# Optimization experiments

Hardware: AMD Instinct MI355X
Metric: run time of the kernel (lower is better)

The kernel has to match this reference:

```python
import jax, jax.numpy as jnp
import numpy as np

EPS = 1e-06


def setup_inputs() -> dict:
    key = jax.random.key(0)
    k1, k2, k3 = jax.random.split(key, 3)
    shape = (64, 1, 480, 640)
    pred = jax.random.normal(k1, shape, dtype=jnp.float32)
    target = jax.random.normal(k2, shape, dtype=jnp.float32)
    valid_mask = jax.random.randint(k3, shape, 0, 2).astype(jnp.bool_)
    return {"pred": pred, "target": target, "valid_mask": valid_mask}


def reference(pred, target, valid_mask):
    B = pred.shape[0]
    mask = valid_mask & jnp.isfinite(pred) & jnp.isfinite(target)
    m = mask.reshape(B, -1)                      # [B, N] bool
    # Zero out invalid entries so non-finite values cannot poison reductions.
    p = jnp.where(m, pred.reshape(B, -1), 0.0)   # [B, N]
    t = jnp.where(m, target.reshape(B, -1), 0.0)  # [B, N]
    mf = m.astype(pred.dtype)

    n = mf.sum(axis=-1)                           # valid count per sample
    sum_p = p.sum(axis=-1)
    sum_t = t.sum(axis=-1)
    sum_p2 = (p * p).sum(axis=-1)
    sum_pt = (p * t).sum(axis=-1)

    det = n * sum_p2 - sum_p * sum_p
    safe = jnp.abs(det) > EPS
    det_safe = jnp.where(safe, det, 1.0)
    a = jnp.where(safe, (n * sum_pt - sum_p * sum_t) / det_safe, 1.0)
    b = jnp.where(safe, (sum_t - a * sum_p) / jnp.maximum(n, 1.0), 0.0)

    # Masked mean absolute residual per sample.
    resid = jnp.abs(a[:, None] * p + b[:, None] - t) * mf
    per_sample = resid.sum(axis=-1) / jnp.maximum(n, 1.0)

    include = (n >= 2.0).astype(pred.dtype)      # samples with < 2 valid px skipped
    cnt = include.sum()
    loss = jnp.where(cnt > 0, (per_sample * include).sum() / jnp.maximum(cnt, 1.0), 0.0)
    return loss
```

## Files before the change

kernel.cpp:

```cpp
#include <hip/hip_runtime.h>

#define B_SAMPLES 64
#define F4PS      76800
#define BPS       30
#define F4PB      2560
#define TPB       256
#define ITERS     10
#define WPB       4
#define EPS_DET   1e-6f

typedef __attribute__((address_space(3))) void       lds_void;
typedef const __attribute__((address_space(1))) void gbl_void;

__device__ __forceinline__ bool finitef(float x) {
    return (__float_as_uint(x) & 0x7f800000u) != 0x7f800000u;
}

__device__ __forceinline__ bool detect_byte_layout(const void* mask, int base4,
                                                   int* sflag) {
    const uint4* m16 =
        (const uint4*)((const unsigned char*)mask + (size_t)base4 * 4);
    uint4 m = m16[threadIdx.x];
    unsigned v = (m.x | m.y | m.z | m.w) & 0xffffff00u;
    if (threadIdx.x == 0) *sflag = 0;
    __syncthreads();
    if (__any(v != 0) && (threadIdx.x & 63) == 0) *sflag = 1;
    __syncthreads();
    return *sflag != 0;
}

__device__ __forceinline__ void stage3(const float4* gp, const float4* gt,
                                       const unsigned* gm,
                                       unsigned char* lbuf) {
    __builtin_amdgcn_global_load_lds((gbl_void*)gp, (lds_void*)lbuf, 16, 0, 0);
    __builtin_amdgcn_global_load_lds((gbl_void*)gt, (lds_void*)(lbuf + 1024),
                                     16, 0, 0);
    __builtin_amdgcn_global_load_lds((gbl_void*)gm, (lds_void*)(lbuf + 2048),
                                     4, 0, 0);
}

__global__ void
sums_kernel(const float* __restrict__ pred, const float* __restrict__ target,
            const void* __restrict__ mask, float* __restrict__ partials) {
    const int s   = blockIdx.x / BPS;
    const int sub = blockIdx.x % BPS;
    const int base4 = s * F4PS + sub * F4PB;
    const int tid = threadIdx.x, lane = tid & 63, w = tid >> 6;

    __shared__ __align__(16) unsigned char stg[WPB][2][2304];
    __shared__ float red[WPB][5];
    __shared__ int sflag;

    const bool byteLayout = detect_byte_layout(mask, base4, &sflag);

    const float4* p4 = (const float4*)pred;
    const float4* t4 = (const float4*)target;

    float n = 0.f, sp = 0.f, st = 0.f, sp2 = 0.f, spt = 0.f;
    auto accum = [&](float p, float t, bool mv) {
        bool ok = mv && finitef(p) && finitef(t);
        float pv = ok ? p : 0.f;
        float tv = ok ? t : 0.f;
        n   += ok ? 1.f : 0.f;
        sp  += pv;
        st  += tv;
        sp2 += pv * pv;
        spt += pv * tv;
    };

    if (byteLayout) {
        const unsigned* m4 = (const unsigned*)mask;
        unsigned char* buf0 = &stg[w][0][0];
        unsigned char* buf1 = &stg[w][1][0];
        const int i0 = base4 + w * 64 + lane;
        stage3(p4 + i0, t4 + i0, m4 + i0, buf0);
#pragma unroll
        for (int t = 0; t < ITERS; ++t) {
            unsigned char* cur = (t & 1) ? buf1 : buf0;
            unsigned char* nxt = (t & 1) ? buf0 : buf1;
            if (t < ITERS - 1) {
                const int i4 = i0 + (t + 1) * TPB;
                stage3(p4 + i4, t4 + i4, m4 + i4, nxt);
                __builtin_amdgcn_sched_barrier(0);
                asm volatile("s_waitcnt vmcnt(3)" ::: "memory");
            } else {
                __builtin_amdgcn_sched_barrier(0);
                asm volatile("s_waitcnt vmcnt(0)" ::: "memory");
            }
            __builtin_amdgcn_sched_barrier(0);
            const float4  pv = *(const float4*)(cur + (size_t)lane * 16);
            const float4  tv = *(const float4*)(cur + 1024 + (size_t)lane * 16);
            const unsigned mm = *(const unsigned*)(cur + 2048 + (size_t)lane * 4);
            accum(pv.x, tv.x, (mm & 0x000000ffu) != 0);
            accum(pv.y, tv.y, (mm & 0x0000ff00u) != 0);
            accum(pv.z, tv.z, (mm & 0x00ff0000u) != 0);
            accum(pv.w, tv.w, (mm & 0xff000000u) != 0);
        }
    } else {
        const int4* m4 = (const int4*)mask;
        for (int t = 0; t < ITERS; ++t) {
            const int i4 = base4 + t * TPB + tid;
            float4 p = p4[i4]; float4 tt = t4[i4]; int4 mm = m4[i4];
            accum(p.x, tt.x, mm.x != 0);
            accum(p.y, tt.y, mm.y != 0);
            accum(p.z, tt.z, mm.z != 0);
            accum(p.w, tt.w, mm.w != 0);
        }
    }

    {
        float vals[5] = {n, sp, st, sp2, spt};
#pragma unroll
        for (int q = 0; q < 5; ++q) {
            float v = vals[q];
#pragma unroll
            for (int off = 32; off; off >>= 1) v += __shfl_xor(v, off);
            if (lane == 0) red[w][q] = v;
        }
        __syncthreads();
        if (tid == 0) {
#pragma unroll
            for (int q = 0; q < 5; ++q)
                partials[(size_t)blockIdx.x * 5 + q] =
                    red[0][q] + red[1][q] + red[2][q] + red[3][q];
        }
    }
}

__global__ void
resid_kernel(const float* __restrict__ pred, const float* __restrict__ target,
             const void* __restrict__ mask, const float* __restrict__ partials,
             float* __restrict__ rpart) {
    const int s   = blockIdx.x / BPS;
    const int sub = blockIdx.x % BPS;
    const int base4 = s * F4PS + sub * F4PB;
    const int tid = threadIdx.x, lane = tid & 63, w = tid >> 6;

    __shared__ __align__(16) unsigned char stg[WPB][2][2304];
    __shared__ float red[WPB];
    __shared__ float s_ab[2];
    __shared__ int sflag;

    const bool byteLayout = detect_byte_layout(mask, base4, &sflag);

    const float4* p4 = (const float4*)pred;
    const float4* t4 = (const float4*)target;
    const unsigned* m4b = (const unsigned*)mask;

    unsigned char* buf0 = &stg[w][0][0];
    unsigned char* buf1 = &stg[w][1][0];
    const int i0 = base4 + w * 64 + lane;
    if (byteLayout)
        stage3(p4 + i0, t4 + i0, m4b + i0, buf0);

    if (tid < 64) {
        float q0 = 0.f, q1 = 0.f, q2 = 0.f, q3 = 0.f, q4 = 0.f;
        if (tid < BPS) {
            const float* q = partials + (size_t)(s * BPS + tid) * 5;
            q0 = q[0]; q1 = q[1]; q2 = q[2]; q3 = q[3]; q4 = q[4];
        }
#pragma unroll
        for (int off = 32; off; off >>= 1) {
            q0 += __shfl_xor(q0, off);
            q1 += __shfl_xor(q1, off);
            q2 += __shfl_xor(q2, off);
            q3 += __shfl_xor(q3, off);
            q4 += __shfl_xor(q4, off);
        }
        if (tid == 0) {
            float det = q0 * q3 - q1 * q1;
            bool safe = fabsf(det) > EPS_DET;
            float a  = safe ? (q0 * q4 - q1 * q2) / det : 1.f;
            float bb = safe ? (q2 - a * q1) / fmaxf(q0, 1.f) : 0.f;
            s_ab[0] = a;
            s_ab[1] = bb;
        }
    }
    __syncthreads();
    const float av = s_ab[0];
    const float bv = s_ab[1];

    float r = 0.f;
    auto raccum = [&](float p, float t, bool mv) {
        bool ok = mv && finitef(p) && finitef(t);
        r += ok ? fabsf(av * p + bv - t) : 0.f;
    };

    if (byteLayout) {
#pragma unroll
        for (int t = 0; t < ITERS; ++t) {
            unsigned char* cur = (t & 1) ? buf1 : buf0;
            unsigned char* nxt = (t & 1) ? buf0 : buf1;
            if (t < ITERS - 1) {
                const int i4 = i0 + (t + 1) * TPB;
                stage3(p4 + i4, t4 + i4, m4b + i4, nxt);
                __builtin_amdgcn_sched_barrier(0);
                asm volatile("s_waitcnt vmcnt(3)" ::: "memory");
            } else {
                __builtin_amdgcn_sched_barrier(0);
                asm volatile("s_waitcnt vmcnt(0)" ::: "memory");
            }
            __builtin_amdgcn_sched_barrier(0);
            const float4  pv = *(const float4*)(cur + (size_t)lane * 16);
            const float4  tv = *(const float4*)(cur + 1024 + (size_t)lane * 16);
            const unsigned mm = *(const unsigned*)(cur + 2048 + (size_t)lane * 4);
            raccum(pv.x, tv.x, (mm & 0x000000ffu) != 0);
            raccum(pv.y, tv.y, (mm & 0x0000ff00u) != 0);
            raccum(pv.z, tv.z, (mm & 0x00ff0000u) != 0);
            raccum(pv.w, tv.w, (mm & 0xff000000u) != 0);
        }
    } else {
        const int4* m4 = (const int4*)mask;
        for (int t = 0; t < ITERS; ++t) {
            const int i4 = base4 + t * TPB + tid;
            float4 p = p4[i4]; float4 tt = t4[i4]; int4 mm = m4[i4];
            raccum(p.x, tt.x, mm.x != 0);
            raccum(p.y, tt.y, mm.y != 0);
            raccum(p.z, tt.z, mm.z != 0);
            raccum(p.w, tt.w, mm.w != 0);
        }
    }

    {
        float v = r;
#pragma unroll
        for (int off = 32; off; off >>= 1) v += __shfl_xor(v, off);
        if (lane == 0) red[w] = v;
        __syncthreads();
        if (tid == 0)
            rpart[blockIdx.x] = red[0] + red[1] + red[2] + red[3];
    }
}

__global__ void final_kernel(const float* __restrict__ partials,
                             const float* __restrict__ rpart,
                             float* __restrict__ out) {
    const int s = threadIdx.x;
    double r = 0, n = 0;
    for (int b = 0; b < BPS; ++b) {
        r += (double)rpart[s * BPS + b];
        n += (double)partials[(size_t)(s * BPS + b) * 5 + 0];
    }
    double per = r / fmax(n, 1.0);
    double inc = (n >= 2.0) ? 1.0 : 0.0;
    double v = per * inc;
#pragma unroll
    for (int off = 32; off; off >>= 1) {
        v += __shfl_down(v, off);
        inc += __shfl_down(inc, off);
    }
    if (s == 0) out[0] = (float)(inc > 0.0 ? v / fmax(inc, 1.0) : 0.0);
}

extern "C" void kernel_launch(void* const* d_in, const int* in_sizes, int n_in,
                              void* d_out, int out_size, void* d_ws, size_t ws_size,
                              hipStream_t stream) {
    const float* pred = (const float*)d_in[0];
    const float* target = (const float*)d_in[1];
    const void* mask = d_in[2];
    float* out = (float*)d_out;

    float* partials = (float*)d_ws;
    float* rpart = partials + (size_t)B_SAMPLES * BPS * 5;

    sums_kernel<<<B_SAMPLES * BPS, TPB, 0, stream>>>(pred, target, mask,
                                                     partials);
    resid_kernel<<<B_SAMPLES * BPS, TPB, 0, stream>>>(pred, target, mask,
                                                      partials, rpart);
    final_kernel<<<1, 64, 0, stream>>>(partials, rpart, out);
}
```

Before: 79.94 us.

## Bit-pack validity mask in first pass and fuse final reduction via ticket

```diff
diff --git a/kernel.cpp b/kernel.cpp
--- a/kernel.cpp
+++ b/kernel.cpp
@@ -3,11 +3,13 @@
 #define B_SAMPLES 64
 #define F4PS      76800
 #define BPS       30
+#define NBLK      (B_SAMPLES * BPS)
 #define F4PB      2560
 #define TPB       256
 #define ITERS     10
 #define WPB       4
 #define EPS_DET   1e-6f
+#define BM_DW     320
 
 typedef __attribute__((address_space(3))) void       lds_void;
 typedef const __attribute__((address_space(1))) void gbl_void;
@@ -30,24 +32,31 @@
 }
 
 __device__ __forceinline__ void stage3(const float4* gp, const float4* gt,
-                                       const unsigned* gm,
+                                       const unsigned* gm, unsigned char* lbuf) {
+    __builtin_amdgcn_global_load_lds((gbl_void*)gp, (lds_void*)lbuf, 16, 0, 0);
+    __builtin_amdgcn_global_load_lds((gbl_void*)gt, (lds_void*)(lbuf + 1024), 16, 0, 0);
+    __builtin_amdgcn_global_load_lds((gbl_void*)gm, (lds_void*)(lbuf + 2048), 4, 0, 0);
+}
+__device__ __forceinline__ void stage2(const float4* gp, const float4* gt,
                                        unsigned char* lbuf) {
     __builtin_amdgcn_global_load_lds((gbl_void*)gp, (lds_void*)lbuf, 16, 0, 0);
-    __builtin_amdgcn_global_load_lds((gbl_void*)gt, (lds_void*)(lbuf + 1024),
-                                     16, 0, 0);
-    __builtin_amdgcn_global_load_lds((gbl_void*)gm, (lds_void*)(lbuf + 2048),
-                                     4, 0, 0);
-}
-
+    __builtin_amdgcn_global_load_lds((gbl_void*)gt, (lds_void*)(lbuf + 1024), 16, 0, 0);
+}
+
+template <bool BITPK>
 __global__ void
 sums_kernel(const float* __restrict__ pred, const float* __restrict__ target,
-            const void* __restrict__ mask, float* __restrict__ partials) {
+            const void* __restrict__ mask, float* __restrict__ partials,
+            unsigned* __restrict__ bitpack, int* __restrict__ ticket) {
     const int s   = blockIdx.x / BPS;
     const int sub = blockIdx.x % BPS;
     const int base4 = s * F4PS + sub * F4PB;
     const int tid = threadIdx.x, lane = tid & 63, w = tid >> 6;
 
+    if (BITPK && blockIdx.x == 0 && tid == 0) *ticket = 0;
+
     __shared__ __align__(16) unsigned char stg[WPB][2][2304];
+    __shared__ unsigned long long bm64[WPB * ITERS * 4];
     __shared__ float red[WPB][5];
     __shared__ int sflag;
 
@@ -57,15 +66,11 @@
     const float4* t4 = (const float4*)target;
 
     float n = 0.f, sp = 0.f, st = 0.f, sp2 = 0.f, spt = 0.f;
-    auto accum = [&](float p, float t, bool mv) {
-        bool ok = mv && finitef(p) && finitef(t);
+    auto acc1 = [&](float p, float t, bool ok) {
         float pv = ok ? p : 0.f;
         float tv = ok ? t : 0.f;
         n   += ok ? 1.f : 0.f;
-        sp  += pv;
-        st  += tv;
-        sp2 += pv * pv;
-        spt += pv * tv;
+        sp  += pv;  st += tv;  sp2 += pv * pv;  spt += pv * tv;
     };
 
     if (byteLayout) {
@@ -91,20 +96,42 @@
             const float4  pv = *(const float4*)(cur + (size_t)lane * 16);
             const float4  tv = *(const float4*)(cur + 1024 + (size_t)lane * 16);
             const unsigned mm = *(const unsigned*)(cur + 2048 + (size_t)lane * 4);
-            accum(pv.x, tv.x, (mm & 0x000000ffu) != 0);
-            accum(pv.y, tv.y, (mm & 0x0000ff00u) != 0);
-            accum(pv.z, tv.z, (mm & 0x00ff0000u) != 0);
-            accum(pv.w, tv.w, (mm & 0xff000000u) != 0);
+            bool o0 = (mm & 0x000000ffu) && finitef(pv.x) && finitef(tv.x);
+            bool o1 = (mm & 0x0000ff00u) && finitef(pv.y) && finitef(tv.y);
+            bool o2 = (mm & 0x00ff0000u) && finitef(pv.z) && finitef(tv.z);
+            bool o3 = (mm & 0xff000000u) && finitef(pv.w) && finitef(tv.w);
+            if (BITPK) {
+                unsigned long long B0 = __ballot(o0), B1 = __ballot(o1);
+                unsigned long long B2 = __ballot(o2), B3 = __ballot(o3);
+                if (lane == 0) {
+                    const int c = (w * ITERS + t) * 4;
+                    bm64[c] = B0; bm64[c + 1] = B1;
+                    bm64[c + 2] = B2; bm64[c + 3] = B3;
+                }
+            }
+            acc1(pv.x, tv.x, o0); acc1(pv.y, tv.y, o1);
+            acc1(pv.z, tv.z, o2); acc1(pv.w, tv.w, o3);
         }
     } else {
         const int4* m4 = (const int4*)mask;
         for (int t = 0; t < ITERS; ++t) {
             const int i4 = base4 + t * TPB + tid;
             float4 p = p4[i4]; float4 tt = t4[i4]; int4 mm = m4[i4];
-            accum(p.x, tt.x, mm.x != 0);
-            accum(p.y, tt.y, mm.y != 0);
-            accum(p.z, tt.z, mm.z != 0);
-            accum(p.w, tt.w, mm.w != 0);
+            bool o0 = mm.x && finitef(p.x) && finitef(tt.x);
+            bool o1 = mm.y && finitef(p.y) && finitef(tt.y);
+            bool o2 = mm.z && finitef(p.z) && finitef(tt.z);
+            bool o3 = mm.w && finitef(p.w) && finitef(tt.w);
+            if (BITPK) {
+                unsigned long long B0 = __ballot(o0), B1 = __ballot(o1);
+                unsigned long long B2 = __ballot(o2), B3 = __ballot(o3);
+                if (lane == 0) {
+                    const int c = (w * ITERS + t) * 4;
+                    bm64[c] = B0; bm64[c + 1] = B1;
+                    bm64[c + 2] = B2; bm64[c + 3] = B3;
+                }
+            }
+            acc1(p.x, tt.x, o0); acc1(p.y, tt.y, o1);
+            acc1(p.z, tt.z, o2); acc1(p.w, tt.w, o3);
         }
     }
 
@@ -125,33 +152,40 @@
                     red[0][q] + red[1][q] + red[2][q] + red[3][q];
         }
     }
-}
-
+    if (BITPK) {
+        const unsigned* bm32 = (const unsigned*)bm64;
+        unsigned* g = bitpack + (size_t)blockIdx.x * BM_DW;
+        g[tid] = bm32[tid];
+        if (tid < BM_DW - TPB) g[TPB + tid] = bm32[TPB + tid];
+    }
+}
+
+template <bool BITPK>
 __global__ void
 resid_kernel(const float* __restrict__ pred, const float* __restrict__ target,
              const void* __restrict__ mask, const float* __restrict__ partials,
-             float* __restrict__ rpart) {
+             float* __restrict__ rpart, const unsigned* __restrict__ bitpack,
+             int* __restrict__ ticket, float* __restrict__ out) {
     const int s   = blockIdx.x / BPS;
     const int sub = blockIdx.x % BPS;
     const int base4 = s * F4PS + sub * F4PB;
     const int tid = threadIdx.x, lane = tid & 63, w = tid >> 6;
 
     __shared__ __align__(16) unsigned char stg[WPB][2][2304];
+    __shared__ unsigned long long bml64[WPB * ITERS * 4];
     __shared__ float red[WPB];
     __shared__ float s_ab[2];
     __shared__ int sflag;
-
-    const bool byteLayout = detect_byte_layout(mask, base4, &sflag);
-
-    const float4* p4 = (const float4*)pred;
-    const float4* t4 = (const float4*)target;
-    const unsigned* m4b = (const unsigned*)mask;
-
-    unsigned char* buf0 = &stg[w][0][0];
-    unsigned char* buf1 = &stg[w][1][0];
-    const int i0 = base4 + w * 64 + lane;
-    if (byteLayout)
-        stage3(p4 + i0, t4 + i0, m4b + i0, buf0);
+    __shared__ int s_last;
+
+    bool byteLayout = true;
+    if (!BITPK) byteLayout = detect_byte_layout(mask, base4, &sflag);
+    if (BITPK) {
+        unsigned* b32 = (unsigned*)bml64;
+        b32[tid] = bitpack[(size_t)blockIdx.x * BM_DW + tid];
+        if (tid < BM_DW - TPB)
+            b32[TPB + tid] = bitpack[(size_t)blockIdx.x * BM_DW + TPB + tid];
+    }
 
     if (tid < 64) {
         float q0 = 0.f, q1 = 0.f, q2 = 0.f, q3 = 0.f, q4 = 0.f;
@@ -161,10 +195,8 @@
         }
 #pragma unroll
         for (int off = 32; off; off >>= 1) {
-            q0 += __shfl_xor(q0, off);
-            q1 += __shfl_xor(q1, off);
-            q2 += __shfl_xor(q2, off);
-            q3 += __shfl_xor(q3, off);
+            q0 += __shfl_xor(q0, off); q1 += __shfl_xor(q1, off);
+            q2 += __shfl_xor(q2, off); q3 += __shfl_xor(q3, off);
             q4 += __shfl_xor(q4, off);
         }
         if (tid == 0) {
@@ -172,28 +204,61 @@
             bool safe = fabsf(det) > EPS_DET;
             float a  = safe ? (q0 * q4 - q1 * q2) / det : 1.f;
             float bb = safe ? (q2 - a * q1) / fmaxf(q0, 1.f) : 0.f;
-            s_ab[0] = a;
-            s_ab[1] = bb;
+            s_ab[0] = a; s_ab[1] = bb;
         }
     }
     __syncthreads();
     const float av = s_ab[0];
     const float bv = s_ab[1];
 
+    const float4* p4 = (const float4*)pred;
+    const float4* t4 = (const float4*)target;
+
     float r = 0.f;
-    auto raccum = [&](float p, float t, bool mv) {
-        bool ok = mv && finitef(p) && finitef(t);
+    auto racc = [&](float p, float t, bool ok) {
         r += ok ? fabsf(av * p + bv - t) : 0.f;
     };
 
-    if (byteLayout) {
+    unsigned char* buf0 = &stg[w][0][0];
+    unsigned char* buf1 = &stg[w][1][0];
+    const int i0 = base4 + w * 64 + lane;
+
+    if (BITPK) {
+        stage2(p4 + i0, t4 + i0, buf0);
 #pragma unroll
         for (int t = 0; t < ITERS; ++t) {
             unsigned char* cur = (t & 1) ? buf1 : buf0;
             unsigned char* nxt = (t & 1) ? buf0 : buf1;
             if (t < ITERS - 1) {
                 const int i4 = i0 + (t + 1) * TPB;
-                stage3(p4 + i4, t4 + i4, m4b + i4, nxt);
+                stage2(p4 + i4, t4 + i4, nxt);
+                __builtin_amdgcn_sched_barrier(0);
+                asm volatile("s_waitcnt vmcnt(2)" ::: "memory");
+            } else {
+                __builtin_amdgcn_sched_barrier(0);
+                asm volatile("s_waitcnt vmcnt(0)" ::: "memory");
+            }
+            __builtin_amdgcn_sched_barrier(0);
+            const float4 pv = *(const float4*)(cur + (size_t)lane * 16);
+            const float4 tv = *(const float4*)(cur + 1024 + (size_t)lane * 16);
+            const int c = (w * ITERS + t) * 4;
+            const unsigned long long B0 = bml64[c],     B1 = bml64[c + 1];
+            const unsigned long long B2 = bml64[c + 2], B3 = bml64[c + 3];
+            racc(pv.x, tv.x, (B0 >> lane) & 1ull);
+            racc(pv.y, tv.y, (B1 >> lane) & 1ull);
+            racc(pv.z, tv.z, (B2 >> lane) & 1ull);
+            racc(pv.w, tv.w, (B3 >> lane) & 1ull);
+        }
+    } else if (byteLayout) {
+        const unsigned* m4 = (const unsigned*)mask;
+        stage3(p4 + i0, t4 + i0, m4 + i0, buf0);
+#pragma unroll
+        for (int t = 0; t < ITERS; ++t) {
+            unsigned char* cur = (t & 1) ? buf1 : buf0;
+            unsigned char* nxt = (t & 1) ? buf0 : buf1;
+            if (t < ITERS - 1) {
+                const int i4 = i0 + (t + 1) * TPB;
+                stage3(p4 + i4, t4 + i4, m4 + i4, nxt);
                 __builtin_amdgcn_sched_barrier(0);
                 asm volatile("s_waitcnt vmcnt(3)" ::: "memory");
             } else {
@@ -204,20 +269,20 @@
             const float4  pv = *(const float4*)(cur + (size_t)lane * 16);
             const float4  tv = *(const float4*)(cur + 1024 + (size_t)lane * 16);
             const unsigned mm = *(const unsigned*)(cur + 2048 + (size_t)lane * 4);
-            raccum(pv.x, tv.x, (mm & 0x000000ffu) != 0);
-            raccum(pv.y, tv.y, (mm & 0x0000ff00u) != 0);
-            raccum(pv.z, tv.z, (mm & 0x00ff0000u) != 0);
-            raccum(pv.w, tv.w, (mm & 0xff000000u) != 0);
+            racc(pv.x, tv.x, (mm & 0x000000ffu) && finitef(pv.x) && finitef(tv.x));
+            racc(pv.y, tv.y, (mm & 0x0000ff00u) && finitef(pv.y) && finitef(tv.y));
+            racc(pv.z, tv.z, (mm & 0x00ff0000u) && finitef(pv.z) && finitef(tv.z));
+            racc(pv.w, tv.w, (mm & 0xff000000u) && finitef(pv.w) && finitef(tv.w));
         }
     } else {
         const int4* m4 = (const int4*)mask;
         for (int t = 0; t < ITERS; ++t) {
             const int i4 = base4 + t * TPB + tid;
             float4 p = p4[i4]; float4 tt = t4[i4]; int4 mm = m4[i4];
-            raccum(p.x, tt.x, mm.x != 0);
-            raccum(p.y, tt.y, mm.y != 0);
-            raccum(p.z, tt.z, mm.z != 0);
-            raccum(p.w, tt.w, mm.w != 0);
+            racc(p.x, tt.x, mm.x && finitef(p.x) && finitef(tt.x));
+            racc(p.y, tt.y, mm.y && finitef(p.y) && finitef(tt.y));
+            racc(p.z, tt.z, mm.z && finitef(p.z) && finitef(tt.z));
+            racc(p.w, tt.w, mm.w && finitef(p.w) && finitef(tt.w));
         }
     }
 
@@ -230,26 +295,40 @@
         if (tid == 0)
             rpart[blockIdx.x] = red[0] + red[1] + red[2] + red[3];
     }
-}
-
-__global__ void final_kernel(const float* __restrict__ partials,
-                             const float* __restrict__ rpart,
-                             float* __restrict__ out) {
-    const int s = threadIdx.x;
-    double r = 0, n = 0;
-    for (int b = 0; b < BPS; ++b) {
-        r += (double)rpart[s * BPS + b];
-        n += (double)partials[(size_t)(s * BPS + b) * 5 + 0];
-    }
-    double per = r / fmax(n, 1.0);
-    double inc = (n >= 2.0) ? 1.0 : 0.0;
-    double v = per * inc;
-#pragma unroll
-    for (int off = 32; off; off >>= 1) {
-        v += __shfl_down(v, off);
-        inc += __shfl_down(inc, off);
-    }
-    if (s == 0) out[0] = (float)(inc > 0.0 ? v / fmax(inc, 1.0) : 0.0);
+
+    __threadfence();
+    if (tid == 0) {
+        int old = atomicAdd(ticket, 1);
+        s_last = (old == NBLK - 1);
+    }
+    __syncthreads();
+    if (s_last) {
+        __threadfence();
+        float* fr = (float*)&stg[0][0][0];
+        float* fn = fr + NBLK;
+        for (int i = tid; i < NBLK; i += TPB) {
+            fr[i] = rpart[i];
+            fn[i] = partials[(size_t)i * 5];
+        }
+        __syncthreads();
+        if (tid < 64) {
+            const int ss = tid;
+            double rr = 0.0, nn = 0.0;
+            for (int b = 0; b < BPS; ++b) {
+                rr += (double)fr[ss * BPS + b];
+                nn += (double)fn[ss * BPS + b];
+            }
+            double per = rr / fmax(nn, 1.0);
+            double inc = (nn >= 2.0) ? 1.0 : 0.0;
+            double v = per * inc;
+#pragma unroll
+            for (int off = 32; off; off >>= 1) {
+                v   += __shfl_down(v, off);
+                inc += __shfl_down(inc, off);
+            }
+            if (ss == 0) out[0] = (float)(inc > 0.0 ? v / fmax(inc, 1.0) : 0.0);
+        }
+    }
 }
 
 extern "C" void kernel_launch(void* const* d_in, const int* in_sizes, int n_in,
@@ -260,12 +339,27 @@
     const void* mask = d_in[2];
     float* out = (float*)d_out;
 
-    float* partials = (float*)d_ws;
-    float* rpart = partials + (size_t)B_SAMPLES * BPS * 5;
-
-    sums_kernel<<<B_SAMPLES * BPS, TPB, 0, stream>>>(pred, target, mask,
-                                                     partials);
-    resid_kernel<<<B_SAMPLES * BPS, TPB, 0, stream>>>(pred, target, mask,
-                                                      partials, rpart);
-    final_kernel<<<1, 64, 0, stream>>>(partials, rpart, out);
-}
+    int* ticket = (int*)d_ws;
+    float* partials = (float*)((char*)d_ws + 64);
+    float* rpart = partials + (size_t)NBLK * 5;
+    unsigned* bitpack = (unsigned*)(rpart + NBLK);
+
+    const size_t need = 64 + (size_t)NBLK * 5 * 4 + (size_t)NBLK * 4 +
+                        (size_t)NBLK * BM_DW * 4;
+    const bool bitpk = ws_size >= need;
+
+    if (bitpk) {
+        sums_kernel<true><<<NBLK, TPB, 0, stream>>>(pred, target, mask,
+                                                    partials, bitpack, ticket);
+        resid_kernel<true><<<NBLK, TPB, 0, stream>>>(pred, target, mask,
+                                                     partials, rpart, bitpack,
+                                                     ticket, out);
+    } else {
+        sums_kernel<false><<<NBLK, TPB, 0, stream>>>(pred, target, mask,
+                                                     partials, bitpack, ticket);
+        hipMemsetAsync(ticket, 0, 4, stream);
+        resid_kernel<false><<<NBLK, TPB, 0, stream>>>(pred, target, mask,
+                                                      partials, rpart, bitpack,
+                                                      ticket, out);
+    }
+}
```

Result: slower. 305.2 us (+281.8%).

## Fuse sums and residual passes into one cooperative kernel with grid sync

Applied to the files above, without the earlier changes.

```diff
diff --git a/kernel.cpp b/kernel.cpp
--- a/kernel.cpp
+++ b/kernel.cpp
@@ -1,8 +1,12 @@
 #include <hip/hip_runtime.h>
+#include <hip/hip_cooperative_groups.h>
+
+namespace cg = cooperative_groups;
 
 #define B_SAMPLES 64
 #define F4PS      76800
 #define BPS       30
+#define NBLK      (B_SAMPLES * BPS)
 #define F4PB      2560
 #define TPB       256
 #define ITERS     10
@@ -30,13 +34,178 @@
 }
 
 __device__ __forceinline__ void stage3(const float4* gp, const float4* gt,
-                                       const unsigned* gm,
-                                       unsigned char* lbuf) {
+                                       const unsigned* gm, unsigned char* lbuf) {
     __builtin_amdgcn_global_load_lds((gbl_void*)gp, (lds_void*)lbuf, 16, 0, 0);
-    __builtin_amdgcn_global_load_lds((gbl_void*)gt, (lds_void*)(lbuf + 1024),
-                                     16, 0, 0);
-    __builtin_amdgcn_global_load_lds((gbl_void*)gm, (lds_void*)(lbuf + 2048),
-                                     4, 0, 0);
+    __builtin_amdgcn_global_load_lds((gbl_void*)gt, (lds_void*)(lbuf + 1024), 16, 0, 0);
+    __builtin_amdgcn_global_load_lds((gbl_void*)gm, (lds_void*)(lbuf + 2048), 4, 0, 0);
+}
+
+__global__ void
+fused(const float* __restrict__ pred, const float* __restrict__ target,
+      const void* __restrict__ mask, float* __restrict__ partials,
+      float* __restrict__ rpart) {
+    const int s   = blockIdx.x / BPS;
+    const int sub = blockIdx.x % BPS;
+    const int base4 = s * F4PS + sub * F4PB;
+    const int tid = threadIdx.x, lane = tid & 63, w = tid >> 6;
+
+    __shared__ __align__(16) unsigned char stg[WPB][2][2304];
+    __shared__ float red[WPB][5];
+    __shared__ float s_ab[2];
+    __shared__ int sflag;
+
+    const bool byteLayout = detect_byte_layout(mask, base4, &sflag);
+
+    const float4* p4 = (const float4*)pred;
+    const float4* t4 = (const float4*)target;
+    const unsigned* m4b = (const unsigned*)mask;
+
+    unsigned char* buf0 = &stg[w][0][0];
+    unsigned char* buf1 = &stg[w][1][0];
+    const int i0 = base4 + w * 64 + lane;
+
+    float n = 0.f, sp = 0.f, st = 0.f, sp2 = 0.f, spt = 0.f;
+    auto acc1 = [&](float p, float t, bool ok) {
+        float pv = ok ? p : 0.f;
+        float tv = ok ? t : 0.f;
+        n   += ok ? 1.f : 0.f;
+        sp  += pv;  st += tv;  sp2 += pv * pv;  spt += pv * tv;
+    };
+
+    if (byteLayout) {
+        stage3(p4 + i0, t4 + i0, m4b + i0, buf0);
+#pragma unroll
+        for (int t = 0; t < ITERS; ++t) {
+            unsigned char* cur = (t & 1) ? buf1 : buf0;
+            unsigned char* nxt = (t & 1) ? buf0 : buf1;
+            if (t < ITERS - 1) {
+                const int i4 = i0 + (t + 1) * TPB;
+                stage3(p4 + i4, t4 + i4, m4b + i4, nxt);
+                __builtin_amdgcn_sched_barrier(0);
+                asm volatile("s_waitcnt vmcnt(3)" ::: "memory");
+            } else {
+                __builtin_amdgcn_sched_barrier(0);
+                asm volatile("s_waitcnt vmcnt(0)" ::: "memory");
+            }
+            __builtin_amdgcn_sched_barrier(0);
+            const float4  pv = *(const float4*)(cur + (size_t)lane * 16);
+            const float4  tv = *(const float4*)(cur + 1024 + (size_t)lane * 16);
+            const unsigned mm = *(const unsigned*)(cur + 2048 + (size_t)lane * 4);
+            acc1(pv.x, tv.x, (mm & 0x000000ffu) && finitef(pv.x) && finitef(tv.x));
+            acc1(pv.y, tv.y, (mm & 0x0000ff00u) && finitef(pv.y) && finitef(tv.y));
+            acc1(pv.z, tv.z, (mm & 0x00ff0000u) && finitef(pv.z) && finitef(tv.z));
+            acc1(pv.w, tv.w, (mm & 0xff000000u) && finitef(pv.w) && finitef(tv.w));
+        }
+    } else {
+        const int4* m4 = (const int4*)mask;
+        for (int t = 0; t < ITERS; ++t) {
+            const int i4 = base4 + t * TPB + tid;
+            float4 p = p4[i4]; float4 tt = t4[i4]; int4 mm = m4[i4];
+            acc1(p.x, tt.x, mm.x && finitef(p.x) && finitef(tt.x));
+            acc1(p.y, tt.y, mm.y && finitef(p.y) && finitef(tt.y));
+            acc1(p.z, tt.z, mm.z && finitef(p.z) && finitef(tt.z));
+            acc1(p.w, tt.w, mm.w && finitef(p.w) && finitef(tt.w));
+        }
+    }
+
+    {
+        float vals[5] = {n, sp, st, sp2, spt};
+#pragma unroll
+        for (int q = 0; q < 5; ++q) {
+            float v = vals[q];
+#pragma unroll
+            for (int off = 32; off; off >>= 1) v += __shfl_xor(v, off);
+            if (lane == 0) red[w][q] = v;
+        }
+        __syncthreads();
+        if (tid == 0) {
+#pragma unroll
+            for (int q = 0; q < 5; ++q)
+                partials[(size_t)blockIdx.x * 5 + q] =
+                    red[0][q] + red[1][q] + red[2][q] + red[3][q];
+        }
+    }
+
+    __threadfence();
+    cg::this_grid().sync();
+    __threadfence();
+
+    if (byteLayout)
+        stage3(p4 + i0, t4 + i0, m4b + i0, buf0);
+
+    if (tid < 64) {
+        float q0 = 0.f, q1 = 0.f, q2 = 0.f, q3 = 0.f, q4 = 0.f;
+        if (tid < BPS) {
+            const float* q = partials + (size_t)(s * BPS + tid) * 5;
+            q0 = q[0]; q1 = q[1]; q2 = q[2]; q3 = q[3]; q4 = q[4];
+        }
+#pragma unroll
+        for (int off = 32; off; off >>= 1) {
+            q0 += __shfl_xor(q0, off); q1 += __shfl_xor(q1, off);
+            q2 += __shfl_xor(q2, off); q3 += __shfl_xor(q3, off);
+            q4 += __shfl_xor(q4, off);
+        }
+        if (tid == 0) {
+            float det = q0 * q3 - q1 * q1;
+            bool safe = fabsf(det) > EPS_DET;
+            float a  = safe ? (q0 * q4 - q1 * q2) / det : 1.f;
+            float bb = safe ? (q2 - a * q1) / fmaxf(q0, 1.f) : 0.f;
+            s_ab[0] = a; s_ab[1] = bb;
+        }
+    }
+    __syncthreads();
+    const float av = s_ab[0];
+    const float bv = s_ab[1];
+
+    float r = 0.f;
+    auto racc = [&](float p, float t, bool ok) {
+        r += ok ? fabsf(av * p + bv - t) : 0.f;
+    };
+
+    if (byteLayout) {
+#pragma unroll
+        for (int t = 0; t < ITERS; ++t) {
+            unsigned char* cur = (t & 1) ? buf1 : buf0;
+            unsigned char* nxt = (t & 1) ? buf0 : buf1;
+            if (t < ITERS - 1) {
+                const int i4 = i0 + (t + 1) * TPB;
+                stage3(p4 + i4, t4 + i4, m4b + i4, nxt);
+                __builtin_amdgcn_sched_barrier(0);
+                asm volatile("s_waitcnt vmcnt(3)" ::: "memory");
+            } else {
+                __builtin_amdgcn_sched_barrier(0);
+                asm volatile("s_waitcnt vmcnt(0)" ::: "memory");
+            }
+            __builtin_amdgcn_sched_barrier(0);
+            const float4  pv = *(const float4*)(cur + (size_t)lane * 16);
+            const float4  tv = *(const float4*)(cur + 1024 + (size_t)lane * 16);
+            const unsigned mm = *(const unsigned*)(cur + 2048 + (size_t)lane * 4);
+            racc(pv.x, tv.x, (mm & 0x000000ffu) && finitef(pv.x) && finitef(tv.x));
+            racc(pv.y, tv.y, (mm & 0x0000ff00u) && finitef(pv.y) && finitef(tv.y));
+            racc(pv.z, tv.z, (mm & 0x00ff0000u) && finitef(pv.z) && finitef(tv.z));
+            racc(pv.w, tv.w, (mm & 0xff000000u) && finitef(pv.w) && finitef(tv.w));
+        }
+    } else {
+        const int4* m4 = (const int4*)mask;
+        for (int t = 0; t < ITERS; ++t) {
+            const int i4 = base4 + t * TPB + tid;
+            float4 p = p4[i4]; float4 tt = t4[i4]; int4 mm = m4[i4];
+            racc(p.x, tt.x, mm.x && finitef(p.x) && finitef(tt.x));
+            racc(p.y, tt.y, mm.y && finitef(p.y) && finitef(tt.y));
+            racc(p.z, tt.z, mm.z && finitef(p.z) && finitef(tt.z));
+            racc(p.w, tt.w, mm.w && finitef(p.w) && finitef(tt.w));
+        }
+    }
+
+    {
+        float v = r;
+#pragma unroll
+        for (int off = 32; off; off >>= 1) v += __shfl_xor(v, off);
+        if (lane == 0) red[w][0] = v;
+        __syncthreads();
+        if (tid == 0)
+            rpart[blockIdx.x] = red[0][0] + red[1][0] + red[2][0] + red[3][0];
+    }
 }
 
 __global__ void
@@ -52,20 +221,15 @@
     __shared__ int sflag;
 
     const bool byteLayout = detect_byte_layout(mask, base4, &sflag);
-
     const float4* p4 = (const float4*)pred;
     const float4* t4 = (const float4*)target;
 
     float n = 0.f, sp = 0.f, st = 0.f, sp2 = 0.f, spt = 0.f;
-    auto accum = [&](float p, float t, bool mv) {
-        bool ok = mv && finitef(p) && finitef(t);
+    auto acc1 = [&](float p, float t, bool ok) {
         float pv = ok ? p : 0.f;
         float tv = ok ? t : 0.f;
-        n   += ok ? 1.f : 0.f;
-        sp  += pv;
-        st  += tv;
-        sp2 += pv * pv;
-        spt += pv * tv;
+        n += ok ? 1.f : 0.f;
+        sp += pv; st += tv; sp2 += pv * pv; spt += pv * tv;
     };
 
     if (byteLayout) {
@@ -91,20 +255,20 @@
             const float4  pv = *(const float4*)(cur + (size_t)lane * 16);
             const float4  tv = *(const float4*)(cur + 1024 + (size_t)lane * 16);
             const unsigned mm = *(const unsigned*)(cur + 2048 + (size_t)lane * 4);
-            accum(pv.x, tv.x, (mm & 0x000000ffu) != 0);
-            accum(pv.y, tv.y, (mm & 0x0000ff00u) != 0);
-            accum(pv.z, tv.z, (mm & 0x00ff0000u) != 0);
-            accum(pv.w, tv.w, (mm & 0xff000000u) != 0);
+            acc1(pv.x, tv.x, (mm & 0x000000ffu) && finitef(pv.x) && finitef(tv.x));
+            acc1(pv.y, tv.y, (mm & 0x0000ff00u) && finitef(pv.y) && finitef(tv.y));
+            acc1(pv.z, tv.z, (mm & 0x00ff0000u) && finitef(pv.z) && finitef(tv.z));
+            acc1(pv.w, tv.w, (mm & 0xff000000u) && finitef(pv.w) && finitef(tv.w));
         }
     } else {
         const int4* m4 = (const int4*)mask;
         for (int t = 0; t < ITERS; ++t) {
             const int i4 = base4 + t * TPB + tid;
             float4 p = p4[i4]; float4 tt = t4[i4]; int4 mm = m4[i4];
-            accum(p.x, tt.x, mm.x != 0);
-            accum(p.y, tt.y, mm.y != 0);
-            accum(p.z, tt.z, mm.z != 0);
-            accum(p.w, tt.w, mm.w != 0);
+            acc1(p.x, tt.x, mm.x && finitef(p.x) && finitef(tt.x));
+            acc1(p.y, tt.y, mm.y && finitef(p.y) && finitef(tt.y));
+            acc1(p.z, tt.z, mm.z && finitef(p.z) && finitef(tt.z));
+            acc1(p.w, tt.w, mm.w && finitef(p.w) && finitef(tt.w));
         }
     }
 
@@ -142,7 +306,6 @@
     __shared__ int sflag;
 
     const bool byteLayout = detect_byte_layout(mask, base4, &sflag);
-
     const float4* p4 = (const float4*)pred;
     const float4* t4 = (const float4*)target;
     const unsigned* m4b = (const unsigned*)mask;
@@ -161,10 +324,8 @@
         }
 #pragma unroll
         for (int off = 32; off; off >>= 1) {
-            q0 += __shfl_xor(q0, off);
-            q1 += __shfl_xor(q1, off);
-            q2 += __shfl_xor(q2, off);
-            q3 += __shfl_xor(q3, off);
+            q0 += __shfl_xor(q0, off); q1 += __shfl_xor(q1, off);
+            q2 += __shfl_xor(q2, off); q3 += __shfl_xor(q3, off);
             q4 += __shfl_xor(q4, off);
         }
         if (tid == 0) {
@@ -172,8 +333,7 @@
             bool safe = fabsf(det) > EPS_DET;
             float a  = safe ? (q0 * q4 - q1 * q2) / det : 1.f;
             float bb = safe ? (q2 - a * q1) / fmaxf(q0, 1.f) : 0.f;
-            s_ab[0] = a;
-            s_ab[1] = bb;
+            s_ab[0] = a; s_ab[1] = bb;
         }
     }
     __syncthreads();
@@ -181,8 +341,7 @@
     const float bv = s_ab[1];
 
     float r = 0.f;
-    auto raccum = [&](float p, float t, bool mv) {
-        bool ok = mv && finitef(p) && finitef(t);
+    auto racc = [&](float p, float t, bool ok) {
         r += ok ? fabsf(av * p + bv - t) : 0.f;
     };
 
@@ -204,20 +363,20 @@
             const float4  pv = *(const float4*)(cur + (size_t)lane * 16);
             const float4  tv = *(const float4*)(cur + 1024 + (size_t)lane * 16);
             const unsigned mm = *(const unsigned*)(cur + 2048 + (size_t)lane * 4);
-            raccum(pv.x, tv.x, (mm & 0x000000ffu) != 0);
-            raccum(pv.y, tv.y, (mm & 0x0000ff00u) != 0);
-            raccum(pv.z, tv.z, (mm & 0x00ff0000u) != 0);
-            raccum(pv.w, tv.w, (mm & 0xff000000u) != 0);
+            racc(pv.x, tv.x, (mm & 0x000000ffu) && finitef(pv.x) && finitef(tv.x));
+            racc(pv.y, tv.y, (mm & 0x0000ff00u) && finitef(pv.y) && finitef(tv.y));
+            racc(pv.z, tv.z, (mm & 0x00ff0000u) && finitef(pv.z) && finitef(tv.z));
+            racc(pv.w, tv.w, (mm & 0xff000000u) && finitef(pv.w) && finitef(tv.w));
         }
     } else {
         const int4* m4 = (const int4*)mask;
         for (int t = 0; t < ITERS; ++t) {
             const int i4 = base4 + t * TPB + tid;
             float4 p = p4[i4]; float4 tt = t4[i4]; int4 mm = m4[i4];
-            raccum(p.x, tt.x, mm.x != 0);
-            raccum(p.y, tt.y, mm.y != 0);
-            raccum(p.z, tt.z, mm.z != 0);
-            raccum(p.w, tt.w, mm.w != 0);
+            racc(p.x, tt.x, mm.x && finitef(p.x) && finitef(tt.x));
+            racc(p.y, tt.y, mm.y && finitef(p.y) && finitef(tt.y));
+            racc(p.z, tt.z, mm.z && finitef(p.z) && finitef(tt.z));
+            racc(p.w, tt.w, mm.w && finitef(p.w) && finitef(tt.w));
         }
     }
 
@@ -261,11 +420,22 @@
     float* out = (float*)d_out;
 
     float* partials = (float*)d_ws;
-    float* rpart = partials + (size_t)B_SAMPLES * BPS * 5;
-
-    sums_kernel<<<B_SAMPLES * BPS, TPB, 0, stream>>>(pred, target, mask,
-                                                     partials);
-    resid_kernel<<<B_SAMPLES * BPS, TPB, 0, stream>>>(pred, target, mask,
-                                                      partials, rpart);
+    float* rpart = partials + (size_t)NBLK * 5;
+
+    int perCU = 0;
+    hipError_t qe =
+        hipOccupancyMaxActiveBlocksPerMultiprocessor(&perCU, fused, TPB, 0);
+    const bool coop = (qe == hipSuccess) && (perCU * 256 >= NBLK);
+
+    if (coop) {
+        void* args[] = {(void*)&pred, (void*)&target, (void*)&mask,
+                        (void*)&partials, (void*)&rpart};
+        hipLaunchCooperativeKernel((const void*)fused, dim3(NBLK), dim3(TPB),
+                                   args, 0, stream);
+    } else {
+        sums_kernel<<<NBLK, TPB, 0, stream>>>(pred, target, mask, partials);
+        resid_kernel<<<NBLK, TPB, 0, stream>>>(pred, target, mask, partials,
+                                               rpart);
+    }
     final_kernel<<<1, 64, 0, stream>>>(partials, rpart, out);
 }
```

New measurement: 82.88 us. 3.7% more time.
